# Kernel optimization log

Measured on AMD Instinct MI355X. Metric: run time of the kernel, lower is better.

The kernel has to match this reference:

```python
import jax, jax.numpy as jnp
import numpy as np
import math

R_ON = 0.05
ALPHA = 0.001  # training-mode alpha (module zeroes it only in eval)


def _fmod(a, b):
    # b/pi * atan(tan(pi*(a/b - 0.5))) + b/2, as in the torch source
    return b / math.pi * jnp.arctan(jnp.tan(math.pi * (a / b - 0.5))) + b / 2


def setup_inputs() -> dict:
    key = jax.random.key(0)
    ks = jax.random.split(key, 7)
    B, T, H = 64, 512, 768
    stdv = 1.0 / math.sqrt(H)
    x = jax.random.normal(ks[0], (B, T, H), dtype=jnp.float32)
    W = jax.random.uniform(ks[1], (4 * H, 4 * H), minval=-stdv, maxval=stdv, dtype=jnp.float32)
    U = jax.random.uniform(ks[2], (4 * H, 4 * H), minval=-stdv, maxval=stdv, dtype=jnp.float32)
    b = jnp.zeros((4 * H,), dtype=jnp.float32)
    w_peep = jax.random.uniform(ks[3], (3 * H,), minval=-stdv, maxval=stdv, dtype=jnp.float32)
    tau = jnp.exp(jax.random.uniform(ks[4], (H,), minval=0.0, maxval=3.0, dtype=jnp.float32))
    shift = jax.random.uniform(ks[5], (H,), minval=0.0, maxval=float(jnp.mean(tau)), dtype=jnp.float32)
    return {"x": x, "W": W, "U": U, "b": b, "w_peep": w_peep, "tau": tau, "shift": shift}


def reference(x, W, U, b, w_peep, tau, shift):
    B, T, H = x.shape
    # x_t.repeat(1,3) @ W[:3H,:3H] == x_t @ (W[:H,:3H] + W[H:2H,:3H] + W[2H:3H,:3H])
    W3 = W[:3 * H, :3 * H]
    U3 = U[:3 * H, :3 * H]
    Wsum = W3[:H] + W3[H:2 * H] + W3[2 * H:3 * H]  # (H, 3H)
    Usum = U3[:H] + U3[H:2 * H] + U3[2 * H:3 * H]  # (H, 3H)
    b3 = b[:3 * H]
    Wc = W[3 * H:4 * H, 3 * H:4 * H]
    Uc = U[3 * H:4 * H, 3 * H:4 * H]
    bc = b[3 * H:4 * H]

    # Phase gate k[t,h]
    times = jnp.arange(T, dtype=jnp.float32)[:, None]  # (T,1) broadcast to (T,H)
    phi = _fmod(times - shift, tau) / (tau + 1e-8)
    k = jnp.where(
        phi < 0.5 * R_ON,
        2.0 * phi / R_ON,
        jnp.where((0.5 * R_ON <= phi) & (phi < R_ON), 2.0 - 2.0 * phi / R_ON, ALPHA * phi),
    )  # (T, H)

    h0 = jnp.zeros((B, H), dtype=x.dtype)
    c0 = jnp.zeros((B, H), dtype=x.dtype)

    def step(carry, inp):
        h, c = carry
        x_t, k_t = inp  # (B,H), (H,)
        c3 = jnp.tile(c, (1, 3))
        gates = x_t @ Wsum + h @ Usum + b3 + w_peep * c3  # (B, 3H)
        i_t = jax.nn.sigmoid(gates[:, :H])
        f_t = jax.nn.sigmoid(gates[:, H:2 * H])
        o_t = jax.nn.sigmoid(gates[:, 2 * H:3 * H])
        gate_c = x_t @ Wc + h @ Uc + bc
        c_prim = f_t * c + i_t * jnp.tanh(gate_c)
        c_new = k_t * c_prim + (1.0 - k_t) * c
        h_prim = jnp.tanh(c_prim) * o_t
        h_new = k_t * h_prim + (1.0 - k_t) * h
        return (h_new, c_new), h_new

    xs = (jnp.transpose(x, (1, 0, 2)), k)  # time-major
    _, h_out = jax.lax.scan(step, (h0, c0), xs)
    return jnp.transpose(h_out, (1, 0, 2))  # (B, T, H)
```

## Files before the change

### kernel.cpp

```cpp
#include <hip/hip_runtime.h>
#include <math.h>


#define HDIM 768
#define BDIM 64
#define TDIM 512
#define G_BLOCKS 96
#define ND 8

typedef float f32x4 __attribute__((ext_vector_type(4)));
typedef float f32x2 __attribute__((ext_vector_type(2)));
typedef __bf16 bf16x8 __attribute__((ext_vector_type(8)));
typedef _Float16 f16x2 __attribute__((ext_vector_type(2)));
typedef int i32x4 __attribute__((ext_vector_type(4)));
typedef int i32x2 __attribute__((ext_vector_type(2)));

#define OFF_FLAGS 0
#define OFF_HBUF0 24576
#define OFF_HBUF1 (24576 + 98304)
#define OFF_KTAB  (24576 + 2*98304)
#define OFF_WT    (OFF_KTAB + (size_t)512*768*4)
#define OFF_XB    (OFF_WT + (size_t)3072*1536*2)
#define WS_NEED_FULL (OFF_XB + (size_t)512*64*768*2)
#define OFF_GX    OFF_XB
#define WS_NEED_GXF32 (OFF_GX + (size_t)32768*3072*4)
#define WS_NEED_GXF16 (OFF_GX + (size_t)32768*3072*2)


__global__ void k_wcomb(const float* __restrict__ W, const float* __restrict__ U,
                        __bf16* __restrict__ WT) {
  __shared__ __bf16 tile[32][33];
  int tk = blockIdx.x % 48;
  int tn = blockIdx.x / 48;
  int tx = threadIdx.x & 31, ty = threadIdx.x >> 5;
  int k0 = tk * 32, n0 = tn * 32;
#pragma unroll
  for (int i = 0; i < 4; ++i) {
    int k = k0 + ty + 8 * i;
    int n = n0 + tx;
    const float* M = (k < 768) ? W : U;
    int r = (k < 768) ? k : k - 768;
    float v;
    if (n < 2304)
      v = M[(size_t)r * 3072 + n] + M[(size_t)(768 + r) * 3072 + n] +
          M[(size_t)(1536 + r) * 3072 + n];
    else
      v = M[(size_t)(2304 + r) * 3072 + n];
    tile[ty + 8 * i][tx] = (__bf16)v;
  }
  __syncthreads();
#pragma unroll
  for (int i = 0; i < 4; ++i) {
    int n = n0 + ty + 8 * i;
    int k = k0 + tx;
    WT[(size_t)n * 1536 + k] = tile[tx][ty + 8 * i];
  }
}

__global__ void k_ktab(const float* __restrict__ tau, const float* __restrict__ shift,
                       float* __restrict__ kT) {
  int idx = blockIdx.x * 256 + threadIdx.x;
  int d = idx % 768, t = idx / 768;
  float bb = tau[d];
  float a = (float)t - shift[d];
  const float PI = 3.14159265358979323846f;
  float fm = bb / PI * atanf(tanf(PI * (a / bb - 0.5f))) + bb * 0.5f;
  float phi = fm / (bb + 1e-8f);
  float kv;
  if (phi < 0.5f * 0.05f)      kv = 2.0f * phi / 0.05f;
  else if (phi < 0.05f)        kv = 2.0f - 2.0f * phi / 0.05f;
  else                         kv = 0.001f * phi;
  kT[idx] = kv;
}

__global__ void k_xb(const float* __restrict__ x, __bf16* __restrict__ xb) {
  int idx = blockIdx.x * 256 + threadIdx.x;
  int k = idx % 768;
  int tb = idx / 768;
  int b = tb % 64, t = tb / 64;
  xb[idx] = (__bf16)x[((size_t)b * 512 + t) * 768 + k];
}

template <int F16OUT>
__global__ __launch_bounds__(256, 2)
void k_xgemm(const float* __restrict__ x, const __bf16* __restrict__ Wt,
             void* __restrict__ Cv) {
  __shared__ __align__(16) unsigned char AsB[128 * 128];
  __shared__ __align__(16) unsigned char BsB[128 * 128];
  const int tid = threadIdx.x;
  const int wave = tid >> 6, lane = tid & 63;
  const int quad = lane >> 4, l15 = lane & 15;
  const int wr = wave >> 1, wc = wave & 1;
  const int mt = blockIdx.x / 24, nt = blockIdx.x % 24;
  const int m0 = mt * 128, n0 = nt * 128;

  f32x4 acc[4][4];
#pragma unroll
  for (int i = 0; i < 4; ++i)
#pragma unroll
    for (int jj = 0; jj < 4; ++jj) acc[i][jj] = (f32x4){0.f, 0.f, 0.f, 0.f};

  for (int kt = 0; kt < 12; ++kt) {
#pragma unroll
    for (int s0 = 0; s0 < 4; ++s0) {
      int s = s0 * 256 + tid;
      int row = s >> 3, part = s & 7;
      int sw = (row & 7) << 4;
      int m = m0 + row;
      const float* ap = x + ((size_t)(m & 63) * 512 + (m >> 6)) * 768 + kt * 64 + part * 8;
      f32x4 a0 = *(const f32x4*)ap;
      f32x4 a1 = *(const f32x4*)(ap + 4);
      bf16x8 av;
#pragma unroll
      for (int q = 0; q < 4; ++q) { av[q] = (__bf16)a0[q]; av[q + 4] = (__bf16)a1[q]; }
      *(bf16x8*)&AsB[row * 128 + ((part * 16) ^ sw)] = av;
      i32x4 vb = *(const i32x4*)((const unsigned char*)Wt +
                                 (size_t)(n0 + row) * 3072 + kt * 128 + part * 16);
      *(i32x4*)&BsB[row * 128 + ((part * 16) ^ sw)] = vb;
    }
    __syncthreads();
#pragma unroll
    for (int ks = 0; ks < 2; ++ks) {
      const int cb = (ks * 32 + quad * 8) * 2;
      bf16x8 af[4], bfr[4];
#pragma unroll
      for (int f = 0; f < 4; ++f) {
        int ar = wr * 64 + f * 16 + l15;
        af[f] = *(const bf16x8*)&AsB[ar * 128 + (cb ^ ((ar & 7) << 4))];
        int br = wc * 64 + f * 16 + l15;
        bfr[f] = *(const bf16x8*)&BsB[br * 128 + (cb ^ ((br & 7) << 4))];
      }
#pragma unroll
      for (int fm = 0; fm < 4; ++fm)
#pragma unroll
        for (int fn = 0; fn < 4; ++fn)
          acc[fm][fn] = __builtin_amdgcn_mfma_f32_16x16x32_bf16(af[fm], bfr[fn],
                                                                acc[fm][fn], 0, 0, 0);
    }
    __syncthreads();
  }
#pragma unroll
  for (int fm = 0; fm < 4; ++fm) {
    int m = m0 + wr * 64 + fm * 16 + quad * 4;
#pragma unroll
    for (int fn = 0; fn < 4; ++fn) {
      int n = n0 + wc * 64 + fn * 16 + l15;
#pragma unroll
      for (int r = 0; r < 4; ++r) {
        if constexpr (F16OUT)
          ((_Float16*)Cv)[(size_t)(m + r) * 3072 + n] = (_Float16)acc[fm][fn][r];
        else
          ((float*)Cv)[(size_t)(m + r) * 3072 + n] = acc[fm][fn][r];
      }
    }
  }
}

__device__ __forceinline__ i32x4 ldg_c16(const void* p) {
  i32x4 r;
  asm volatile("global_load_dwordx4 %0, %1, off sc0 sc1" : "=v"(r) : "v"(p));
  return r;
}
__device__ __forceinline__ i32x2 ldg_n8(const void* p) {
  i32x2 r;
  asm volatile("global_load_dwordx2 %0, %1, off" : "=v"(r) : "v"(p));
  return r;
}
__device__ __forceinline__ int ldg_n4(const void* p) {
  int r;
  asm volatile("global_load_dword %0, %1, off" : "=v"(r) : "v"(p));
  return r;
}
__device__ __forceinline__ void stg_c4(void* p, int v) {
  asm volatile("global_store_dword %0, %1, off sc0 sc1"
               :: "v"(p), "v"(v) : "memory");
}
__device__ __forceinline__ void stg_n8(void* p, i32x2 v) {
  asm volatile("global_store_dwordx2 %0, %1, off"
               :: "v"(p), "v"(v) : "memory");
}
__device__ __forceinline__ void waitcnt_vm0() {
  asm volatile("s_waitcnt vmcnt(0)" ::: "memory");
}
#define HOLD4(x) asm volatile("" : "+v"(x))
#define HOLD2(x) asm volatile("" : "+v"(x))
#define HOLDI(x) asm volatile("" : "+v"(x))

#define HSTEP(i, VMS)                                                         \
  asm volatile("s_waitcnt vmcnt(" VMS ")");                                   \
  HOLD4(hr[i][0]); HOLD4(hr[i][1]); HOLD4(hr[i][2]); HOLD4(hr[i][3]);         \
  { const int kc = 96 + (wave * 6 + (i)) * 4 + quad;                          \
    bf16x8 b0 = *(const bf16x8*)&Bl2[(size_t)(kc * 32 + l15) * 8];            \
    bf16x8 b1 = *(const bf16x8*)&Bl2[(size_t)(kc * 32 + 16 + l15) * 8];       \
    _Pragma("unroll")                                                         \
    for (int rt = 0; rt < 4; ++rt) {                                          \
      bf16x8 av = __builtin_bit_cast(bf16x8, hr[i][rt]);                      \
      acc[rt][0] = __builtin_amdgcn_mfma_f32_16x16x32_bf16(av, b0, acc[rt][0], 0, 0, 0); \
      acc[rt][1] = __builtin_amdgcn_mfma_f32_16x16x32_bf16(av, b1, acc[rt][1], 0, 0, 0); \
    } }

template <int MODE>
__global__ __launch_bounds__(256, 1)
void k_lstm(const __bf16* __restrict__ xb, const float* __restrict__ xf,
            const void* __restrict__ gxv,
            const __bf16* __restrict__ WT, const float* __restrict__ kT,
            const float* __restrict__ bias, const float* __restrict__ wpeep,
            __bf16* h0buf, __bf16* h1buf, float* __restrict__ out, int* flags) {
  const int j = blockIdx.x, d0 = j * ND;
  const int tid = threadIdx.x;
  const int wave = tid >> 6, lane = tid & 63;
  const int quad = lane >> 4, l15 = lane & 15;

  __shared__ __align__(16) __bf16 Bl2[192 * 32 * 8];
  __shared__ float gacc2[4][32][68];

  for (int idx = tid; idx < 6144; idx += 256) {
    int c = idx & 31, kc = idx >> 5;
    int n = (c >> 3) * 768 + d0 + (c & 7);
    *(bf16x8*)&Bl2[(size_t)idx * 8] = *(const bf16x8*)&WT[(size_t)n * 1536 + kc * 8];
  }

  const int dq = tid & 3, bb = tid >> 2;
  const int ed0 = d0 + dq * 2;
  const f32x2 bi2  = *(const f32x2*)&bias[ed0];
  const f32x2 bf2  = *(const f32x2*)&bias[768 + ed0];
  const f32x2 bo2  = *(const f32x2*)&bias[1536 + ed0];
  const f32x2 bc2  = *(const f32x2*)&bias[2304 + ed0];
  const f32x2 wpi2 = *(const f32x2*)&wpeep[ed0];
  const f32x2 wpf2 = *(const f32x2*)&wpeep[768 + ed0];
  const f32x2 wpo2 = *(const f32x2*)&wpeep[1536 + ed0];

  const int fid0 = wave * 96 + lane;
  const int fid1 = wave * 96 + 64 + (lane & 31);
  const int* fp0 = flags + fid0 * 16;
  const int* fp1 = flags + fid1 * 16;

  f32x2 creg; creg[0] = 0.f; creg[1] = 0.f;
  f32x2 hreg; hreg[0] = 0.f; hreg[1] = 0.f;

  __syncthreads();

  for (int t = 0; t < TDIM; ++t) {
    const __bf16* hcur = (t & 1) ? h1buf : h0buf;
    __bf16* hnxt = (t & 1) ? h0buf : h1buf;

    i32x2 ktraw = ldg_n8(kT + (size_t)t * 768 + ed0);
    i32x2 gx8[4];
    int   gx4[4];
    if constexpr (MODE == 2) {
#pragma unroll
      for (int g = 0; g < 4; ++g)
        gx8[g] = ldg_n8((const float*)gxv + ((size_t)(t * 64 + bb)) * 3072 + g * 768 + ed0);
    } else if constexpr (MODE == 3) {
#pragma unroll
      for (int g = 0; g < 4; ++g)
        gx4[g] = ldg_n4((const _Float16*)gxv + ((size_t)(t * 64 + bb)) * 3072 + g * 768 + ed0);
    }

    f32x4 acc[4][2];
#pragma unroll
    for (int rt = 0; rt < 4; ++rt) {
      acc[rt][0] = (f32x4){0.f, 0.f, 0.f, 0.f};
      acc[rt][1] = (f32x4){0.f, 0.f, 0.f, 0.f};
    }

    if constexpr (MODE < 2) {
#pragma unroll
      for (int i = 0; i < 6; ++i) {
        const int kk = (wave * 6 + i) * 32 + quad * 8;
        const int kc = kk >> 3;
        bf16x8 a[4];
        if constexpr (MODE == 1) {
#pragma unroll
          for (int rt = 0; rt < 4; ++rt)
            a[rt] = *(const bf16x8*)(xb + ((size_t)(t * 64 + rt * 16 + l15)) * 768 + kk);
        } else {
#pragma unroll
          for (int rt = 0; rt < 4; ++rt)
#pragma unroll
            for (int q = 0; q < 8; ++q)
              a[rt][q] = (__bf16)xf[((size_t)(rt * 16 + l15) * 512 + t) * 768 + kk + q];
        }
        bf16x8 b0 = *(const bf16x8*)&Bl2[(size_t)(kc * 32 + l15) * 8];
        bf16x8 b1 = *(const bf16x8*)&Bl2[(size_t)(kc * 32 + 16 + l15) * 8];
#pragma unroll
        for (int rt = 0; rt < 4; ++rt) {
          acc[rt][0] = __builtin_amdgcn_mfma_f32_16x16x32_bf16(a[rt], b0, acc[rt][0], 0, 0, 0);
          acc[rt][1] = __builtin_amdgcn_mfma_f32_16x16x32_bf16(a[rt], b1, acc[rt][1], 0, 0, 0);
        }
      }
    }

    for (;;) {
      int v0, v1;
      asm volatile("global_load_dword %0, %2, off sc0 sc1\n\t"
                   "global_load_dword %1, %3, off sc0 sc1\n\t"
                   "s_waitcnt vmcnt(0)"
                   : "=v"(v0), "=v"(v1) : "v"(fp0), "v"(fp1) : "memory");
      if (__all(v0 >= t && v1 >= t)) break;
      __builtin_amdgcn_s_sleep(1);
    }
    HOLD2(ktraw);
    if constexpr (MODE == 2) { HOLD2(gx8[0]); HOLD2(gx8[1]); HOLD2(gx8[2]); HOLD2(gx8[3]); }
    if constexpr (MODE == 3) { HOLDI(gx4[0]); HOLDI(gx4[1]); HOLDI(gx4[2]); HOLDI(gx4[3]); }

    i32x4 hr[6][4];
#pragma unroll
    for (int i = 0; i < 6; ++i) {
      const int hoff = (wave * 6 + i) * 32 + quad * 8;
#pragma unroll
      for (int rt = 0; rt < 4; ++rt)
        hr[i][rt] = ldg_c16(hcur + (size_t)(rt * 16 + l15) * 768 + hoff);
    }
    HSTEP(0, "20")
    HSTEP(1, "16")
    HSTEP(2, "12")
    HSTEP(3, "8")
    HSTEP(4, "4")
    HSTEP(5, "0")

#pragma unroll
    for (int rt = 0; rt < 4; ++rt) {
      *(f32x4*)&gacc2[wave][l15][rt * 16 + quad * 4]      = acc[rt][0];
      *(f32x4*)&gacc2[wave][16 + l15][rt * 16 + quad * 4] = acc[rt][1];
    }
    __syncthreads();

    f32x2 kt2 = __builtin_bit_cast(f32x2, ktraw);
    float gs[2][4];
#pragma unroll
    for (int dd = 0; dd < 2; ++dd)
#pragma unroll
      for (int g = 0; g < 4; ++g) {
        float s = 0.f;
#pragma unroll
        for (int w = 0; w < 4; ++w) s += gacc2[w][g * 8 + dq * 2 + dd][bb];
        if constexpr (MODE == 2)
          s += __builtin_bit_cast(f32x2, gx8[g])[dd];
        if constexpr (MODE == 3)
          s += (float)__builtin_bit_cast(f16x2, gx4[g])[dd];
        gs[dd][g] = s;
      }
    f32x2 cnv, hnv;
#pragma unroll
    for (int dd = 0; dd < 2; ++dd) {
      float c_prev = creg[dd], h_prev = hreg[dd], kt = kt2[dd];
      float gi = gs[dd][0] + bi2[dd] + wpi2[dd] * c_prev;
      float gf = gs[dd][1] + bf2[dd] + wpf2[dd] * c_prev;
      float go = gs[dd][2] + bo2[dd] + wpo2[dd] * c_prev;
      float gc = gs[dd][3] + bc2[dd];
      float iv = 1.f / (1.f + expf(-gi));
      float fv = 1.f / (1.f + expf(-gf));
      float ov = 1.f / (1.f + expf(-go));
      float cp = fv * c_prev + iv * tanhf(gc);
      float cn = kt * cp + (1.f - kt) * c_prev;
      float hp = tanhf(cp) * ov;
      float hn = kt * hp + (1.f - kt) * h_prev;
      cnv[dd] = cn; hnv[dd] = hn;
    }
    creg = cnv; hreg = hnv;

    __bf16 h0 = (__bf16)hnv[0], h1 = (__bf16)hnv[1];
    unsigned hu = (unsigned)__builtin_bit_cast(unsigned short, h0) |
                  ((unsigned)__builtin_bit_cast(unsigned short, h1) << 16);
    stg_c4(hnxt + (size_t)bb * 768 + ed0, (int)hu);
    waitcnt_vm0();
    if (lane == 0) stg_c4(flags + (j * 4 + wave) * 16, t + 1);
    __syncthreads();
    f32x2 ov2; ov2[0] = hnv[0]; ov2[1] = hnv[1];
    stg_n8(out + ((size_t)bb * 512 + t) * 768 + ed0, __builtin_bit_cast(i32x2, ov2));
  }
}

extern "C" void kernel_launch(void* const* d_in, const int* in_sizes, int n_in,
                              void* d_out, int out_size, void* d_ws, size_t ws_size,
                              hipStream_t stream) {
  const float* x     = (const float*)d_in[0];
  const float* W     = (const float*)d_in[1];
  const float* U     = (const float*)d_in[2];
  const float* bias  = (const float*)d_in[3];
  const float* wpeep = (const float*)d_in[4];
  const float* tau   = (const float*)d_in[5];
  const float* shift = (const float*)d_in[6];
  float* out = (float*)d_out;
  char* ws = (char*)d_ws;

  int*    flags = (int*)(ws + OFF_FLAGS);
  __bf16* hb0 = (__bf16*)(ws + OFF_HBUF0);
  __bf16* hb1 = (__bf16*)(ws + OFF_HBUF1);
  float*  kT  = (float*)(ws + OFF_KTAB);
  __bf16* WT  = (__bf16*)(ws + OFF_WT);
  __bf16* xb  = (__bf16*)(ws + OFF_XB);
  void*   gxp = (void*)(ws + OFF_GX);

  int mode;
  if      (ws_size >= WS_NEED_GXF32) mode = 2;
  else if (ws_size >= WS_NEED_GXF16) mode = 3;
  else if (ws_size >= WS_NEED_FULL)  mode = 1;
  else                               mode = 0;

  hipMemsetAsync(ws, 0, OFF_KTAB, stream);
  k_wcomb<<<48 * 96, 256, 0, stream>>>(W, U, WT);
  k_ktab<<<(512 * 768) / 256, 256, 0, stream>>>(tau, shift, kT);

  if (mode == 2) {
    k_xgemm<0><<<256 * 24, 256, 0, stream>>>(x, WT, gxp);
    k_lstm<2><<<G_BLOCKS, 256, 0, stream>>>(nullptr, x, gxp, WT, kT, bias, wpeep,
                                            hb0, hb1, out, flags);
  } else if (mode == 3) {
    k_xgemm<1><<<256 * 24, 256, 0, stream>>>(x, WT, gxp);
    k_lstm<3><<<G_BLOCKS, 256, 0, stream>>>(nullptr, x, gxp, WT, kT, bias, wpeep,
                                            hb0, hb1, out, flags);
  } else if (mode == 1) {
    k_xb<<<(512 * 64 * 768) / 256, 256, 0, stream>>>(x, xb);
    k_lstm<1><<<G_BLOCKS, 256, 0, stream>>>(xb, x, nullptr, WT, kT, bias, wpeep,
                                            hb0, hb1, out, flags);
  } else {
    k_lstm<0><<<G_BLOCKS, 256, 0, stream>>>(nullptr, x, nullptr, WT, kT, bias, wpeep,
                                            hb0, hb1, out, flags);
  }
}
```

Before: 3.477 ms.

## Restructure per-step flag polling, move barrier earlier, and use fast transcendentals

In the precomputed-input modes, the first half of the shared-memory weight staging is skipped, since only the recurrent half is used. Each step now issues the flag poll together with the step's own flag store, so the next step can skip the spin loop when peers are already done. The per-step gate and k loads move after the wait, the block barrier moves to right after the shared reduction, and sigmoid/tanh use __expf/__fdividef. This cuts inter-block synchronization latency on the sequential critical path, at the cost of slightly less accurate activations and a more delicate memory-ordering protocol.

```diff
diff --git a/kernel.cpp b/kernel.cpp
--- a/kernel.cpp
+++ b/kernel.cpp
@@ -182,9 +182,25 @@
 __device__ __forceinline__ void waitcnt_vm0() {
   asm volatile("s_waitcnt vmcnt(0)" ::: "memory");
 }
+__device__ __forceinline__ void ldg_c4_pair_nowait(const void* a, const void* b,
+                                                   int& r0, int& r1) {
+  asm volatile("global_load_dword %0, %2, off sc0 sc1\n\t"
+               "global_load_dword %1, %3, off sc0 sc1"
+               : "=v"(r0), "=v"(r1) : "v"(a), "v"(b) : "memory");
+}
+__device__ __forceinline__ void waitcnt_vm0_pin2(int& a, int& b) {
+  asm volatile("s_waitcnt vmcnt(0)" : "+v"(a), "+v"(b) :: "memory");
+}
 #define HOLD4(x) asm volatile("" : "+v"(x))
 #define HOLD2(x) asm volatile("" : "+v"(x))
 #define HOLDI(x) asm volatile("" : "+v"(x))
+
+__device__ __forceinline__ float sigm_f(float x) {
+  return __fdividef(1.f, 1.f + __expf(-x));
+}
+__device__ __forceinline__ float tanh_f(float x) {
+  return 1.f - __fdividef(2.f, __expf(2.f * x) + 1.f);
+}
 
 #define HSTEP(i, VMS)                                                         \
   asm volatile("s_waitcnt vmcnt(" VMS ")");                                   \
@@ -214,7 +230,7 @@
   __shared__ __align__(16) __bf16 Bl2[192 * 32 * 8];
   __shared__ float gacc2[4][32][68];
 
-  for (int idx = tid; idx < 6144; idx += 256) {
+  for (int idx = tid + (MODE >= 2 ? 3072 : 0); idx < 6144; idx += 256) {
     int c = idx & 31, kc = idx >> 5;
     int n = (c >> 3) * 768 + d0 + (c & 7);
     *(bf16x8*)&Bl2[(size_t)idx * 8] = *(const bf16x8*)&WT[(size_t)n * 1536 + kc * 8];
@@ -238,24 +254,13 @@
   f32x2 creg; creg[0] = 0.f; creg[1] = 0.f;
   f32x2 hreg; hreg[0] = 0.f; hreg[1] = 0.f;
 
+  int ready = 0;
+
   __syncthreads();
 
   for (int t = 0; t < TDIM; ++t) {
     const __bf16* hcur = (t & 1) ? h1buf : h0buf;
     __bf16* hnxt = (t & 1) ? h0buf : h1buf;
-
-    i32x2 ktraw = ldg_n8(kT + (size_t)t * 768 + ed0);
-    i32x2 gx8[4];
-    int   gx4[4];
-    if constexpr (MODE == 2) {
-#pragma unroll
-      for (int g = 0; g < 4; ++g)
-        gx8[g] = ldg_n8((const float*)gxv + ((size_t)(t * 64 + bb)) * 3072 + g * 768 + ed0);
-    } else if constexpr (MODE == 3) {
-#pragma unroll
-      for (int g = 0; g < 4; ++g)
-        gx4[g] = ldg_n4((const _Float16*)gxv + ((size_t)(t * 64 + bb)) * 3072 + g * 768 + ed0);
-    }
 
     f32x4 acc[4][2];
 #pragma unroll
@@ -291,18 +296,30 @@
       }
     }
 
-    for (;;) {
-      int v0, v1;
-      asm volatile("global_load_dword %0, %2, off sc0 sc1\n\t"
-                   "global_load_dword %1, %3, off sc0 sc1\n\t"
-                   "s_waitcnt vmcnt(0)"
-                   : "=v"(v0), "=v"(v1) : "v"(fp0), "v"(fp1) : "memory");
-      if (__all(v0 >= t && v1 >= t)) break;
-      __builtin_amdgcn_s_sleep(1);
-    }
-    HOLD2(ktraw);
-    if constexpr (MODE == 2) { HOLD2(gx8[0]); HOLD2(gx8[1]); HOLD2(gx8[2]); HOLD2(gx8[3]); }
-    if constexpr (MODE == 3) { HOLDI(gx4[0]); HOLDI(gx4[1]); HOLDI(gx4[2]); HOLDI(gx4[3]); }
+    if (MODE < 2 || !ready) {
+      for (;;) {
+        int v0, v1;
+        asm volatile("global_load_dword %0, %2, off sc0 sc1\n\t"
+                     "global_load_dword %1, %3, off sc0 sc1\n\t"
+                     "s_waitcnt vmcnt(0)"
+                     : "=v"(v0), "=v"(v1) : "v"(fp0), "v"(fp1) : "memory");
+        if (__all(v0 >= t && v1 >= t)) break;
+        __builtin_amdgcn_s_sleep(1);
+      }
+    }
+
+    i32x2 ktraw = ldg_n8(kT + (size_t)t * 768 + ed0);
+    i32x2 gx8[4];
+    int   gx4[4];
+    if constexpr (MODE == 2) {
+#pragma unroll
+      for (int g = 0; g < 4; ++g)
+        gx8[g] = ldg_n8((const float*)gxv + ((size_t)(t * 64 + bb)) * 3072 + g * 768 + ed0);
+    } else if constexpr (MODE == 3) {
+#pragma unroll
+      for (int g = 0; g < 4; ++g)
+        gx4[g] = ldg_n4((const _Float16*)gxv + ((size_t)(t * 64 + bb)) * 3072 + g * 768 + ed0);
+    }
 
     i32x4 hr[6][4];
 #pragma unroll
@@ -318,6 +335,9 @@
     HSTEP(3, "8")
     HSTEP(4, "4")
     HSTEP(5, "0")
+    HOLD2(ktraw);
+    if constexpr (MODE == 2) { HOLD2(gx8[0]); HOLD2(gx8[1]); HOLD2(gx8[2]); HOLD2(gx8[3]); }
+    if constexpr (MODE == 3) { HOLDI(gx4[0]); HOLDI(gx4[1]); HOLDI(gx4[2]); HOLDI(gx4[3]); }
 
 #pragma unroll
     for (int rt = 0; rt < 4; ++rt) {
@@ -341,6 +361,8 @@
           s += (float)__builtin_bit_cast(f16x2, gx4[g])[dd];
         gs[dd][g] = s;
       }
+    __syncthreads();
+
     f32x2 cnv, hnv;
 #pragma unroll
     for (int dd = 0; dd < 2; ++dd) {
@@ -349,12 +371,12 @@
       float gf = gs[dd][1] + bf2[dd] + wpf2[dd] * c_prev;
       float go = gs[dd][2] + bo2[dd] + wpo2[dd] * c_prev;
       float gc = gs[dd][3] + bc2[dd];
-      float iv = 1.f / (1.f + expf(-gi));
-      float fv = 1.f / (1.f + expf(-gf));
-      float ov = 1.f / (1.f + expf(-go));
-      float cp = fv * c_prev + iv * tanhf(gc);
+      float iv = sigm_f(gi);
+      float fv = sigm_f(gf);
+      float ov = sigm_f(go);
+      float cp = fv * c_prev + iv * tanh_f(gc);
       float cn = kt * cp + (1.f - kt) * c_prev;
-      float hp = tanhf(cp) * ov;
+      float hp = tanh_f(cp) * ov;
       float hn = kt * hp + (1.f - kt) * h_prev;
       cnv[dd] = cn; hnv[dd] = hn;
     }
@@ -364,11 +386,18 @@
     unsigned hu = (unsigned)__builtin_bit_cast(unsigned short, h0) |
                   ((unsigned)__builtin_bit_cast(unsigned short, h1) << 16);
     stg_c4(hnxt + (size_t)bb * 768 + ed0, (int)hu);
-    waitcnt_vm0();
-    if (lane == 0) stg_c4(flags + (j * 4 + wave) * 16, t + 1);
-    __syncthreads();
     f32x2 ov2; ov2[0] = hnv[0]; ov2[1] = hnv[1];
     stg_n8(out + ((size_t)bb * 512 + t) * 768 + ed0, __builtin_bit_cast(i32x2, ov2));
+    if constexpr (MODE >= 2) {
+      int p0, p1;
+      ldg_c4_pair_nowait(fp0, fp1, p0, p1);
+      waitcnt_vm0_pin2(p0, p1);
+      if (lane == 0) stg_c4(flags + (j * 4 + wave) * 16, t + 1);
+      ready = __all(p0 >= t + 1 && p1 >= t + 1);
+    } else {
+      waitcnt_vm0();
+      if (lane == 0) stg_c4(flags + (j * 4 + wave) * 16, t + 1);
+    }
   }
 }
 
```

Result: slower. 4.079 ms (+17.3%).
